# Performance work log

Hardware: AMD Instinct MI355X
Metric: run time of the kernel (lower is better)

The kernel has to match this reference:

```python
import jax, jax.numpy as jnp
import numpy as np

NUM_CAPSULE = 16
DIM_CAPSULE = 64
ROUTINGS = 3
T_EPS = 1e-7


def setup_inputs() -> dict:
    key = jax.random.key(0)
    k1, k2 = jax.random.split(key)
    x = jax.random.normal(k1, (64, 512, 768), dtype=jnp.float32)
    # xavier-normal-ish init for W: [1, input_dim_capsule, num_capsule*dim_capsule]
    fan_in, fan_out = 768, NUM_CAPSULE * DIM_CAPSULE
    std = float(np.sqrt(2.0 / (fan_in + fan_out)))
    W = jax.random.normal(k2, (1, 768, NUM_CAPSULE * DIM_CAPSULE), dtype=jnp.float32) * std
    return {"x": x, "W": W}


def _squash(v, eps=T_EPS):
    # NOTE: this module's 'squash' is pure L2 normalization with eps, not the
    # classic (s^2/(1+s^2)) squash.
    s2 = jnp.sum(v * v, axis=-1, keepdims=True)
    return v / jnp.sqrt(s2 + eps)


def reference(x, W):
    B, In, _ = x.shape
    # u_hat: [B, In, num*dim] -> [B, num, In, dim]
    u = jnp.matmul(x, W).reshape(B, In, NUM_CAPSULE, DIM_CAPSULE).transpose(0, 2, 1, 3)
    b = jnp.zeros((B, NUM_CAPSULE, In), dtype=u.dtype)  # routing logits
    outputs = None
    for i in range(ROUTINGS):
        # torch code softmaxes over the num_capsule axis (after permute dance)
        c = jax.nn.softmax(b, axis=1)  # [B, num, In]
        outputs = _squash(jnp.einsum('bij,bijk->bik', c, u))  # [B, num, dim]
        if i < ROUTINGS - 1:
            b = jnp.einsum('bik,bijk->bij', outputs, u)  # [B, num, In]
    return outputs
```

## Files before the change

kernel.cpp:

```cpp
#include <hip/hip_runtime.h>
#include <hip/hip_bf16.h>
#include <stdint.h>

#define BATCH 64
#define IN_CAPS 512
#define NCAP 16
#define DCAP 64
#define GN (NCAP * DCAP)
#define GM (BATCH * IN_CAPS)
#define GK 768

typedef __bf16 bf16;
typedef __attribute__((ext_vector_type(8))) __bf16 bf16x8;
typedef __attribute__((ext_vector_type(4))) float f32x4;

__device__ inline void async16(const bf16* g, bf16* l) {
    __builtin_amdgcn_global_load_lds(
        (__attribute__((address_space(1))) void*)g,
        (__attribute__((address_space(3))) void*)l, 16, 0, 0);
}

__global__ __launch_bounds__(256) void k_convX2(const float* __restrict__ X,
                                                bf16* __restrict__ Xb,
                                                float* __restrict__ XS) {
    __shared__ float ls[GK];
    const int tid = threadIdx.x;
    ls[tid] = 0.f; ls[tid + 256] = 0.f; ls[tid + 512] = 0.f;
    __syncthreads();
    const size_t base = (size_t)blockIdx.x * (32 * GK);
    float acc[3][8] = {};
#pragma unroll
    for (int r = 0; r < 12; ++r) {
        const int off = r * 2048 + tid * 8;
        const f32x4 a0 = *(const f32x4*)(X + base + off);
        const f32x4 a1 = *(const f32x4*)(X + base + off + 4);
        bf16x8 o;
        o[0] = (bf16)a0[0]; o[1] = (bf16)a0[1]; o[2] = (bf16)a0[2]; o[3] = (bf16)a0[3];
        o[4] = (bf16)a1[0]; o[5] = (bf16)a1[1]; o[6] = (bf16)a1[2]; o[7] = (bf16)a1[3];
        *(bf16x8*)(Xb + base + off) = o;
        const int g = r % 3;
        acc[g][0] += a0[0]; acc[g][1] += a0[1];
        acc[g][2] += a0[2]; acc[g][3] += a0[3];
        acc[g][4] += a1[0]; acc[g][5] += a1[1];
        acc[g][6] += a1[2]; acc[g][7] += a1[3];
    }
    if (XS != nullptr) {
#pragma unroll
        for (int g = 0; g < 3; ++g) {
            const int cg = (g == 1) ? 512 : (g == 2) ? 256 : 0;
            const int kb = (tid * 8 + cg) % GK;
#pragma unroll
            for (int j = 0; j < 8; ++j) atomicAdd(&ls[kb + j], acc[g][j]);
        }
        __syncthreads();
        const int bidx = blockIdx.x >> 4;
        atomicAdd(&XS[(size_t)bidx * GK + tid],       ls[tid]);
        atomicAdd(&XS[(size_t)bidx * GK + tid + 256], ls[tid + 256]);
        atomicAdd(&XS[(size_t)bidx * GK + tid + 512], ls[tid + 512]);
    }
}

__global__ void k_transW(const float* __restrict__ W, bf16* __restrict__ Wt,
                         float* __restrict__ XS) {
    __shared__ bf16 t[32][33];
    const int k0 = blockIdx.x * 32;
    const int n0 = blockIdx.y * 32;
    const int tx = threadIdx.x, ty = threadIdx.y;
    if (XS != nullptr) {
        const int gid = (blockIdx.y * gridDim.x + blockIdx.x) * 256 + ty * 32 + tx;
        if (gid < BATCH * GK) XS[gid] = 0.f;
    }
#pragma unroll
    for (int r = 0; r < 4; ++r)
        t[ty + r * 8][tx] = (bf16)W[(size_t)(k0 + ty + r * 8) * GN + n0 + tx];
    __syncthreads();
#pragma unroll
    for (int r = 0; r < 4; ++r)
        Wt[(size_t)(n0 + ty + r * 8) * GK + k0 + tx] = t[tx][ty + r * 8];
}

__global__ __launch_bounds__(256) void k_out1(const float* __restrict__ XS,
                                              const float* __restrict__ W,
                                              float* __restrict__ O1) {
    __shared__ float xs[4][GK];
    __shared__ float red[4][4][64];
    const int cap = blockIdx.x & 15;
    const int bg = blockIdx.x >> 4;
    const int tid = threadIdx.x;
    const int k = tid & 63, kq = tid >> 6;
#pragma unroll
    for (int bb = 0; bb < 4; ++bb) {
        const size_t b = (size_t)(bg * 4 + bb);
        xs[bb][tid]       = XS[b * GK + tid];
        xs[bb][tid + 256] = XS[b * GK + tid + 256];
        xs[bb][tid + 512] = XS[b * GK + tid + 512];
    }
    __syncthreads();
    float acc4[4] = {0.f, 0.f, 0.f, 0.f};
    const float* wp = W + (size_t)(kq * 192) * GN + cap * 64 + k;
#pragma unroll 4
    for (int kk = 0; kk < 192; ++kk) {
        const float w = wp[(size_t)kk * GN];
        const int kx = kq * 192 + kk;
        acc4[0] += xs[0][kx] * w;
        acc4[1] += xs[1][kx] * w;
        acc4[2] += xs[2][kx] * w;
        acc4[3] += xs[3][kx] * w;
    }
#pragma unroll
    for (int bb = 0; bb < 4; ++bb) red[bb][kq][k] = acc4[bb];
    __syncthreads();
    if (tid < 64) {
#pragma unroll
        for (int bb = 0; bb < 4; ++bb) {
            float s = (red[bb][0][tid] + red[bb][1][tid] +
                       red[bb][2][tid] + red[bb][3][tid]) * 0.0625f;
            float ss = s * s;
#pragma unroll
            for (int off = 32; off >= 1; off >>= 1) ss += __shfl_xor(ss, off);
            O1[((size_t)(bg * 4 + bb) * NCAP + cap) * DCAP + tid] =
                s * rsqrtf(ss + 1e-7f);
        }
    }
}

__global__ __launch_bounds__(256) void k_gemm_async(const bf16* __restrict__ Xb,
                                                    const bf16* __restrict__ Wt,
                                                    const float* __restrict__ O1,
                                                    bf16* __restrict__ U,
                                                    float* __restrict__ BL) {
    __shared__ bf16 sA[128 * 32];
    __shared__ bf16 sB[128 * 32];

    const int tid = threadIdx.x;
    const int lane = tid & 63;
    const int wave = tid >> 6;
    const int wm = wave >> 1, wn = wave & 1;
    const int m0 = blockIdx.x * 128;
    const int n0 = blockIdx.y * 128;

    const int c0 = wave * 2, c1 = wave * 2 + 1;
    const int rl = lane >> 2, cl = (lane & 3) * 8;
    const bf16* gA0 = Xb + (size_t)(m0 + c0 * 16 + rl) * GK + cl;
    const bf16* gA1 = Xb + (size_t)(m0 + c1 * 16 + rl) * GK + cl;
    const bf16* gB0 = Wt + (size_t)(n0 + c0 * 16 + rl) * GK + cl;
    const bf16* gB1 = Wt + (size_t)(n0 + c1 * 16 + rl) * GK + cl;
    bf16* lA0 = sA + c0 * 512;
    bf16* lA1 = sA + c1 * 512;
    bf16* lB0 = sB + c0 * 512;
    bf16* lB1 = sB + c1 * 512;

    f32x4 acc[4][4] = {};
    const int fr = lane & 15;
    const int fq = lane >> 4;

    for (int kt = 0; kt < GK / 32; ++kt) {
        __syncthreads();
        async16(gA0, lA0);
        async16(gA1, lA1);
        async16(gB0, lB0);
        async16(gB1, lB1);
        gA0 += 32; gA1 += 32; gB0 += 32; gB1 += 32;
        __syncthreads();

        bf16x8 af[4], bfr[4];
#pragma unroll
        for (int mi = 0; mi < 4; ++mi)
            af[mi] = *(const bf16x8*)(sA + (wm * 64 + mi * 16 + fr) * 32 + fq * 8);
#pragma unroll
        for (int ni = 0; ni < 4; ++ni)
            bfr[ni] = *(const bf16x8*)(sB + (wn * 64 + ni * 16 + fr) * 32 + fq * 8);
#pragma unroll
        for (int mi = 0; mi < 4; ++mi)
#pragma unroll
            for (int ni = 0; ni < 4; ++ni)
                acc[mi][ni] = __builtin_amdgcn_mfma_f32_16x16x32_bf16(
                    af[mi], bfr[ni], acc[mi][ni], 0, 0, 0);
    }

#pragma unroll
    for (int mi = 0; mi < 4; ++mi) {
#pragma unroll
        for (int ni = 0; ni < 4; ++ni) {
#pragma unroll
            for (int r = 0; r < 4; ++r) {
                const int m = m0 + wm * 64 + mi * 16 + fq * 4 + r;
                const int n = n0 + wn * 64 + ni * 16 + fr;
                const int bb = m >> 9, j = m & 511;
                const int ci = n >> 6, k = n & 63;
                U[(((size_t)(bb * NCAP + ci)) * IN_CAPS + j) * DCAP + k] =
                    (bf16)acc[mi][ni][r];
            }
        }
    }

    if (O1 != nullptr) {
        const int b = m0 >> 9;
        const int cap = (n0 >> 6) + wn;
        float o1v[4];
#pragma unroll
        for (int ni = 0; ni < 4; ++ni)
            o1v[ni] = O1[(size_t)b * GN + n0 + wn * 64 + ni * 16 + fr];
#pragma unroll
        for (int mi = 0; mi < 4; ++mi) {
#pragma unroll
            for (int r = 0; r < 4; ++r) {
                float p = o1v[0] * acc[mi][0][r] + o1v[1] * acc[mi][1][r] +
                          o1v[2] * acc[mi][2][r] + o1v[3] * acc[mi][3][r];
                p += __shfl_xor(p, 1);
                p += __shfl_xor(p, 2);
                p += __shfl_xor(p, 4);
                p += __shfl_xor(p, 8);
                if (fr == 0) {
                    const int j = (m0 & 511) + wm * 64 + mi * 16 + fq * 4 + r;
                    BL[((size_t)(b * NCAP + cap)) * IN_CAPS + j] = p;
                }
            }
        }
    }
}

__global__ __launch_bounds__(256) void k_gemm_inline(const float* __restrict__ X,
                                                     const bf16* __restrict__ Wt,
                                                     bf16* __restrict__ U) {
    __shared__ bf16 sA[128 * 32];
    __shared__ bf16 sB[128 * 32];
    const int tid = threadIdx.x;
    const int lane = tid & 63;
    const int wave = tid >> 6;
    const int wm = wave >> 1, wn = wave & 1;
    const int m0 = blockIdx.x * 128;
    const int n0 = blockIdx.y * 128;
    const int srow = tid >> 2;
    const int scol = (tid & 3) * 8;
    f32x4 acc[4][4] = {};
    const int fr = lane & 15;
    const int fq = lane >> 4;
    for (int kt = 0; kt < GK / 32; ++kt) {
        const int kb = kt * 32;
        bf16x8 a0, a1, b0, b1;
        {
            const float* p = X + (size_t)(m0 + srow) * GK + kb + scol;
            const f32x4 x0 = *(const f32x4*)p, x1 = *(const f32x4*)(p + 4);
            const float* q = X + (size_t)(m0 + srow + 64) * GK + kb + scol;
            const f32x4 y0 = *(const f32x4*)q, y1 = *(const f32x4*)(q + 4);
#pragma unroll
            for (int c = 0; c < 4; ++c) {
                a0[c] = (bf16)x0[c]; a0[c + 4] = (bf16)x1[c];
                a1[c] = (bf16)y0[c]; a1[c + 4] = (bf16)y1[c];
            }
        }
        b0 = *(const bf16x8*)(Wt + (size_t)(n0 + srow) * GK + kb + scol);
        b1 = *(const bf16x8*)(Wt + (size_t)(n0 + srow + 64) * GK + kb + scol);
        __syncthreads();
        *(bf16x8*)(sA + srow * 32 + scol) = a0;
        *(bf16x8*)(sA + (srow + 64) * 32 + scol) = a1;
        *(bf16x8*)(sB + srow * 32 + scol) = b0;
        *(bf16x8*)(sB + (srow + 64) * 32 + scol) = b1;
        __syncthreads();
        bf16x8 af[4], bfr[4];
#pragma unroll
        for (int mi = 0; mi < 4; ++mi)
            af[mi] = *(const bf16x8*)(sA + (wm * 64 + mi * 16 + fr) * 32 + fq * 8);
#pragma unroll
        for (int ni = 0; ni < 4; ++ni)
            bfr[ni] = *(const bf16x8*)(sB + (wn * 64 + ni * 16 + fr) * 32 + fq * 8);
#pragma unroll
        for (int mi = 0; mi < 4; ++mi)
#pragma unroll
            for (int ni = 0; ni < 4; ++ni)
                acc[mi][ni] = __builtin_amdgcn_mfma_f32_16x16x32_bf16(
                    af[mi], bfr[ni], acc[mi][ni], 0, 0, 0);
    }
#pragma unroll
    for (int mi = 0; mi < 4; ++mi) {
#pragma unroll
        for (int ni = 0; ni < 4; ++ni) {
#pragma unroll
            for (int r = 0; r < 4; ++r) {
                const int m = m0 + wm * 64 + mi * 16 + fq * 4 + r;
                const int n = n0 + wn * 64 + ni * 16 + fr;
                const int bb = m >> 9, j = m & 511;
                const int ci = n >> 6, k = n & 63;
                U[(((size_t)(bb * NCAP + ci)) * IN_CAPS + j) * DCAP + k] =
                    (bf16)acc[mi][ni][r];
            }
        }
    }
}

__global__ __launch_bounds__(256) void k_route(const bf16* __restrict__ U,
                                               float* __restrict__ BL,
                                               float* __restrict__ OutC,
                                               int mode) {
    __shared__ float sc[IN_CAPS];
    __shared__ float red2[4][64];
    __shared__ float sout[64];
    const int bi = blockIdx.x;
    const int b = bi >> 4, cap = bi & 15;
    const int tid = threadIdx.x;
    const int lane = tid & 63;
    const int wave = tid >> 6;
    const size_t ubase = (size_t)bi * IN_CAPS * DCAP;

    if (mode == 0) {
        sc[tid] = 0.0625f;
        sc[tid + 256] = 0.0625f;
    } else {
#pragma unroll
        for (int h = 0; h < 2; ++h) {
            const int j = tid + h * 256;
            const float* p = BL + (size_t)b * NCAP * IN_CAPS + j;
            float v[16], mx = -1e30f;
#pragma unroll
            for (int i = 0; i < 16; ++i) {
                v[i] = p[(size_t)i * IN_CAPS];
                mx = fmaxf(mx, v[i]);
            }
            float s = 0.f;
#pragma unroll
            for (int i = 0; i < 16; ++i) s += __expf(v[i] - mx);
            sc[j] = __expf(v[cap] - mx) / s;
        }
    }
    __syncthreads();

    const int g = tid & 7;
    const int jr = tid >> 3;

    float acc[8] = {};
#pragma unroll
    for (int it = 0; it < 16; ++it) {
        const int j = it * 32 + jr;
        const bf16x8 v = *(const bf16x8*)(U + ubase + (size_t)it * 2048 + tid * 8);
        const float cv = sc[j];
#pragma unroll
        for (int c = 0; c < 8; ++c) acc[c] += cv * (float)v[c];
    }
#pragma unroll
    for (int c = 0; c < 8; ++c) {
        acc[c] += __shfl_xor(acc[c], 8);
        acc[c] += __shfl_xor(acc[c], 16);
        acc[c] += __shfl_xor(acc[c], 32);
    }
    if ((lane >> 3) == 0) {
#pragma unroll
        for (int c = 0; c < 8; ++c) red2[wave][lane * 8 + c] = acc[c];
    }
    __syncthreads();

    if (tid < 64) {
        float s = red2[0][tid] + red2[1][tid] + red2[2][tid] + red2[3][tid];
        float ss = s * s;
#pragma unroll
        for (int off = 32; off >= 1; off >>= 1) ss += __shfl_xor(ss, off);
        const float val = s * rsqrtf(ss + 1e-7f);
        sout[tid] = val;
        if (mode == 2) OutC[(size_t)bi * DCAP + tid] = val;
    }
    if (mode == 2) return;
    __syncthreads();

    const f32x4 o0 = *(const f32x4*)(sout + g * 8);
    const f32x4 o1 = *(const f32x4*)(sout + g * 8 + 4);
#pragma unroll
    for (int it = 0; it < 16; ++it) {
        const int j = it * 32 + jr;
        const bf16x8 v = *(const bf16x8*)(U + ubase + (size_t)it * 2048 + tid * 8);
        float p = o0[0] * (float)v[0] + o0[1] * (float)v[1] +
                  o0[2] * (float)v[2] + o0[3] * (float)v[3] +
                  o1[0] * (float)v[4] + o1[1] * (float)v[5] +
                  o1[2] * (float)v[6] + o1[3] * (float)v[7];
        p += __shfl_xor(p, 1);
        p += __shfl_xor(p, 2);
        p += __shfl_xor(p, 4);
        if (g == 0) BL[((size_t)b * NCAP + cap) * IN_CAPS + j] = p;
    }
}

extern "C" void kernel_launch(void* const* d_in, const int* in_sizes, int n_in,
                              void* d_out, int out_size, void* d_ws, size_t ws_size,
                              hipStream_t stream) {
    const float* X = (const float*)d_in[0];
    const float* W = (const float*)d_in[1];
    float* OutC = (float*)d_out;

    const size_t u_bytes = (size_t)BATCH * NCAP * IN_CAPS * DCAP * sizeof(bf16);
    const size_t xb_bytes = (size_t)GM * GK * sizeof(bf16);
    const size_t wt_bytes = (size_t)GN * GK * sizeof(bf16);
    const size_t bl_bytes = (size_t)BATCH * NCAP * IN_CAPS * sizeof(float);
    const size_t xs_bytes = (size_t)BATCH * GK * sizeof(float);
    const size_t o1_bytes = (size_t)BATCH * GN * sizeof(float);
    char* ws = (char*)d_ws;

    const size_t need_full = u_bytes + xb_bytes + wt_bytes + bl_bytes + xs_bytes + o1_bytes;
    const size_t need_async = u_bytes + xb_bytes + wt_bytes + bl_bytes;
    const size_t need_small = u_bytes + wt_bytes + bl_bytes;

    bf16* U = (bf16*)ws;

    if (ws_size >= need_full) {
        bf16* Xb = (bf16*)(ws + u_bytes);
        bf16* Wt = (bf16*)(ws + u_bytes + xb_bytes);
        float* BL = (float*)(ws + u_bytes + xb_bytes + wt_bytes);
        float* XS = (float*)(ws + u_bytes + xb_bytes + wt_bytes + bl_bytes);
        float* O1 = (float*)(ws + u_bytes + xb_bytes + wt_bytes + bl_bytes + xs_bytes);
        k_transW<<<dim3(GK / 32, GN / 32), dim3(32, 8), 0, stream>>>(W, Wt, XS);
        k_convX2<<<GM / 32, 256, 0, stream>>>(X, Xb, XS);
        k_out1<<<256, 256, 0, stream>>>(XS, W, O1);
        k_gemm_async<<<dim3(GM / 128, GN / 128), 256, 0, stream>>>(Xb, Wt, O1, U, BL);
        k_route<<<BATCH * NCAP, 256, 0, stream>>>(U, BL, OutC, 1);
        k_route<<<BATCH * NCAP, 256, 0, stream>>>(U, BL, OutC, 2);
    } else if (ws_size >= need_async) {
        bf16* Xb = (bf16*)(ws + u_bytes);
        bf16* Wt = (bf16*)(ws + u_bytes + xb_bytes);
        float* BL = (float*)(ws + u_bytes + xb_bytes + wt_bytes);
        k_transW<<<dim3(GK / 32, GN / 32), dim3(32, 8), 0, stream>>>(W, Wt, nullptr);
        k_convX2<<<GM / 32, 256, 0, stream>>>(X, Xb, nullptr);
        k_gemm_async<<<dim3(GM / 128, GN / 128), 256, 0, stream>>>(Xb, Wt, nullptr, U, BL);
        k_route<<<BATCH * NCAP, 256, 0, stream>>>(U, BL, OutC, 0);
        k_route<<<BATCH * NCAP, 256, 0, stream>>>(U, BL, OutC, 1);
        k_route<<<BATCH * NCAP, 256, 0, stream>>>(U, BL, OutC, 2);
    } else if (ws_size >= need_small) {
        bf16* Wt = (bf16*)(ws + u_bytes);
        float* BL = (float*)(ws + u_bytes + wt_bytes);
        k_transW<<<dim3(GK / 32, GN / 32), dim3(32, 8), 0, stream>>>(W, Wt, nullptr);
        k_gemm_inline<<<dim3(GM / 128, GN / 128), 256, 0, stream>>>(X, Wt, U);
        k_route<<<BATCH * NCAP, 256, 0, stream>>>(U, BL, OutC, 0);
        k_route<<<BATCH * NCAP, 256, 0, stream>>>(U, BL, OutC, 1);
        k_route<<<BATCH * NCAP, 256, 0, stream>>>(U, BL, OutC, 2);
    }
}
```

Baseline: 295.7 us.

## Fuse last two routing iterations into one cooperative kernel with grid sync

Replaces the two separate routing kernel launches with a single cooperative kernel. Each block keeps its slice of U in registers across both iterations and writes intermediate logits to a scratch buffer. A grid-wide sync separates the two iterations. This removes one launch and one full re-read of U from memory, at the cost of the grid sync overhead and the requirement that all 1024 blocks be co-resident (4 per CU). It falls back to the old two-launch path if the occupancy check or the cooperative launch fails.

```diff
diff --git a/kernel.cpp b/kernel.cpp
--- a/kernel.cpp
+++ b/kernel.cpp
@@ -1,6 +1,9 @@
 #include <hip/hip_runtime.h>
+#include <hip/hip_cooperative_groups.h>
 #include <hip/hip_bf16.h>
 #include <stdint.h>
+
+namespace cg = cooperative_groups;
 
 #define BATCH 64
 #define IN_CAPS 512
@@ -9,6 +12,7 @@
 #define GN (NCAP * DCAP)
 #define GM (BATCH * IN_CAPS)
 #define GK 768
+#define NUM_CU 256
 
 typedef __bf16 bf16;
 typedef __attribute__((ext_vector_type(8))) __bf16 bf16x8;
@@ -47,8 +51,8 @@
     if (XS != nullptr) {
 #pragma unroll
         for (int g = 0; g < 3; ++g) {
-            const int cg = (g == 1) ? 512 : (g == 2) ? 256 : 0;
-            const int kb = (tid * 8 + cg) % GK;
+            const int cg2 = (g == 1) ? 512 : (g == 2) ? 256 : 0;
+            const int kb = (tid * 8 + cg2) % GK;
 #pragma unroll
             for (int j = 0; j < 8; ++j) atomicAdd(&ls[kb + j], acc[g][j]);
         }
@@ -289,6 +293,127 @@
     }
 }
 
+__global__ __launch_bounds__(256, 4) void k_route_coop(const bf16* __restrict__ U,
+                                                       const float* __restrict__ BLin,
+                                                       float* __restrict__ BLtmp,
+                                                       float* __restrict__ OutC) {
+    __shared__ float sc[IN_CAPS];
+    __shared__ float red2[4][64];
+    __shared__ float sout[64];
+    const int bi = blockIdx.x;
+    const int b = bi >> 4, cap = bi & 15;
+    const int tid = threadIdx.x;
+    const int lane = tid & 63;
+    const int wave = tid >> 6;
+    const int g = tid & 7;
+    const int jr = tid >> 3;
+    const size_t ubase = (size_t)bi * IN_CAPS * DCAP;
+
+#pragma unroll
+    for (int h = 0; h < 2; ++h) {
+        const int j = tid + h * 256;
+        const float* p = BLin + (size_t)b * NCAP * IN_CAPS + j;
+        float mx = -1e30f;
+#pragma unroll
+        for (int i = 0; i < 16; ++i) mx = fmaxf(mx, p[(size_t)i * IN_CAPS]);
+        float s = 0.f;
+#pragma unroll
+        for (int i = 0; i < 16; ++i) s += __expf(p[(size_t)i * IN_CAPS] - mx);
+        sc[j] = __expf(p[(size_t)cap * IN_CAPS] - mx) / s;
+    }
+    __syncthreads();
+
+    bf16x8 ur[16];
+    float acc[8] = {};
+#pragma unroll
+    for (int it = 0; it < 16; ++it) {
+        ur[it] = *(const bf16x8*)(U + ubase + (size_t)it * 2048 + tid * 8);
+        const float cv = sc[it * 32 + jr];
+#pragma unroll
+        for (int c = 0; c < 8; ++c) acc[c] += cv * (float)ur[it][c];
+    }
+#pragma unroll
+    for (int c = 0; c < 8; ++c) {
+        acc[c] += __shfl_xor(acc[c], 8);
+        acc[c] += __shfl_xor(acc[c], 16);
+        acc[c] += __shfl_xor(acc[c], 32);
+    }
+    if ((lane >> 3) == 0) {
+#pragma unroll
+        for (int c = 0; c < 8; ++c) red2[wave][lane * 8 + c] = acc[c];
+    }
+    __syncthreads();
+    if (tid < 64) {
+        float s = red2[0][tid] + red2[1][tid] + red2[2][tid] + red2[3][tid];
+        float ss = s * s;
+#pragma unroll
+        for (int off = 32; off >= 1; off >>= 1) ss += __shfl_xor(ss, off);
+        sout[tid] = s * rsqrtf(ss + 1e-7f);
+    }
+    __syncthreads();
+
+    {
+        const f32x4 o0 = *(const f32x4*)(sout + g * 8);
+        const f32x4 o1 = *(const f32x4*)(sout + g * 8 + 4);
+#pragma unroll
+        for (int it = 0; it < 16; ++it) {
+            const bf16x8 v = ur[it];
+            float p = o0[0] * (float)v[0] + o0[1] * (float)v[1] +
+                      o0[2] * (float)v[2] + o0[3] * (float)v[3] +
+                      o1[0] * (float)v[4] + o1[1] * (float)v[5] +
+                      o1[2] * (float)v[6] + o1[3] * (float)v[7];
+            p += __shfl_xor(p, 1);
+            p += __shfl_xor(p, 2);
+            p += __shfl_xor(p, 4);
+            if (g == 0)
+                BLtmp[((size_t)(b * NCAP + cap)) * IN_CAPS + it * 32 + jr] = p;
+        }
+    }
+
+    __threadfence();
+    cg::this_grid().sync();
+
+#pragma unroll
+    for (int h = 0; h < 2; ++h) {
+        const int j = tid + h * 256;
+        const float* p = BLtmp + (size_t)b * NCAP * IN_CAPS + j;
+        float mx = -1e30f;
+#pragma unroll
+        for (int i = 0; i < 16; ++i) mx = fmaxf(mx, p[(size_t)i * IN_CAPS]);
+        float s = 0.f;
+#pragma unroll
+        for (int i = 0; i < 16; ++i) s += __expf(p[(size_t)i * IN_CAPS] - mx);
+        sc[j] = __expf(p[(size_t)cap * IN_CAPS] - mx) / s;
+    }
+    __syncthreads();
+
+    float acc2[8] = {};
+#pragma unroll
+    for (int it = 0; it < 16; ++it) {
+        const float cv = sc[it * 32 + jr];
+#pragma unroll
+        for (int c = 0; c < 8; ++c) acc2[c] += cv * (float)ur[it][c];
+    }
+#pragma unroll
+    for (int c = 0; c < 8; ++c) {
+        acc2[c] += __shfl_xor(acc2[c], 8);
+        acc2[c] += __shfl_xor(acc2[c], 16);
+        acc2[c] += __shfl_xor(acc2[c], 32);
+    }
+    if ((lane >> 3) == 0) {
+#pragma unroll
+        for (int c = 0; c < 8; ++c) red2[wave][lane * 8 + c] = acc2[c];
+    }
+    __syncthreads();
+    if (tid < 64) {
+        float s = red2[0][tid] + red2[1][tid] + red2[2][tid] + red2[3][tid];
+        float ss = s * s;
+#pragma unroll
+        for (int off = 32; off >= 1; off >>= 1) ss += __shfl_xor(ss, off);
+        OutC[(size_t)bi * DCAP + tid] = s * rsqrtf(ss + 1e-7f);
+    }
+}
+
 __global__ __launch_bounds__(256) void k_route(const bf16* __restrict__ U,
                                                float* __restrict__ BL,
                                                float* __restrict__ OutC,
@@ -409,8 +534,24 @@
         k_convX2<<<GM / 32, 256, 0, stream>>>(X, Xb, XS);
         k_out1<<<256, 256, 0, stream>>>(XS, W, O1);
         k_gemm_async<<<dim3(GM / 128, GN / 128), 256, 0, stream>>>(Xb, Wt, O1, U, BL);
-        k_route<<<BATCH * NCAP, 256, 0, stream>>>(U, BL, OutC, 1);
-        k_route<<<BATCH * NCAP, 256, 0, stream>>>(U, BL, OutC, 2);
+
+        float* BLtmp = (float*)Xb;
+        int maxBlk = 0;
+        hipError_t oe = hipOccupancyMaxActiveBlocksPerMultiprocessor(
+            &maxBlk, k_route_coop, 256, 0);
+        bool coop_ok = false;
+        if (oe == hipSuccess && maxBlk >= 4) {
+            const bf16* Uc = U;
+            const float* BLc = BL;
+            void* kargs[] = {(void*)&Uc, (void*)&BLc, (void*)&BLtmp, (void*)&OutC};
+            hipError_t le = hipLaunchCooperativeKernel(
+                k_route_coop, dim3(BATCH * NCAP), dim3(256), kargs, 0, stream);
+            coop_ok = (le == hipSuccess);
+        }
+        if (!coop_ok) {
+            k_route<<<BATCH * NCAP, 256, 0, stream>>>(U, BL, OutC, 1);
+            k_route<<<BATCH * NCAP, 256, 0, stream>>>(U, BL, OutC, 2);
+        }
     } else if (ws_size >= need_async) {
         bf16* Xb = (bf16*)(ws + u_bytes);
         bf16* Wt = (bf16*)(ws + u_bytes + xb_bytes);
```

Result: no change. 296.6 us (+0.3%).
